# Performance work log

Hardware: AMD Instinct MI355X
Metric: run time of the kernel (lower is better)

## Reference

```python
import jax, jax.numpy as jnp
import numpy as np

NEG_INF = -1e30  # used via float('-inf') in original; -inf literal is fine too


def setup_inputs() -> dict:
    key = jax.random.key(0)
    kq, kk, kv = jax.random.split(key, 3)
    b, h, s, d = 2, 32, 2048, 128
    q = jax.random.normal(kq, (b, h, s, d), dtype=jnp.float32)
    k = jax.random.normal(kk, (b, h, s, d), dtype=jnp.float32)
    v = jax.random.normal(kv, (b, h, s, d), dtype=jnp.float32)
    # causal mask, True = masked (matches the module's `~tril` path when mask is None)
    mask = ~jnp.tril(jnp.ones((s, s), dtype=bool))
    attention_mask = jnp.broadcast_to(mask[None, None], (b, 1, s, s))
    return {"query_layer": q, "key_layer": k, "value_layer": v,
            "attention_mask": attention_mask}


def reference(query_layer, key_layer, value_layer, attention_mask):
    b, h, sq, hd = query_layer.shape
    norm_factor = jnp.sqrt(jnp.asarray(hd, dtype=query_layer.dtype))
    # scores: [b, h, sq, sk], computed in fp32 as in the original (.float())
    scores = jnp.einsum('bhqd,bhkd->bhqk', query_layer, key_layer) / norm_factor
    scores = scores.astype(jnp.float32)
    scores = jnp.where(attention_mask, -jnp.inf, scores)
    probs = jax.nn.softmax(scores, axis=-1).astype(value_layer.dtype)
    # context: [b, h, sq, hd]
    ctx = jnp.einsum('bhqk,bhkd->bhqd', probs, value_layer)
    # -> [b, sq, h*hd]
    ctx = jnp.transpose(ctx, (0, 2, 1, 3)).reshape(b, sq, h * hd)
    return ctx
```

## Files before the change

kernel.cpp:

```cpp
#include <hip/hip_runtime.h>
#include <hip/hip_bf16.h>

typedef __attribute__((ext_vector_type(8))) short bf16x8;
typedef __attribute__((ext_vector_type(8))) unsigned short u16x8;
typedef __attribute__((ext_vector_type(4))) float f32x4;

#define S_LEN 2048
#define D_DIM 128
#define BH_NUM 64
#define OUT_W 4096

__device__ __forceinline__ unsigned short f2bf(float f){
  unsigned int u = __float_as_uint(f);
  u += 0x7FFFu + ((u >> 16) & 1u);
  return (unsigned short)(u >> 16);
}

__device__ __forceinline__ short pbf(float f){
  __hip_bfloat16 h = __float2bfloat16(f);
  return *reinterpret_cast<short*>(&h);
}

__device__ __forceinline__ void gl_lds16(const void* g, void* l){
  __builtin_amdgcn_global_load_lds(
      (const __attribute__((address_space(1))) unsigned int*)g,
      (__attribute__((address_space(3))) unsigned int*)l, 16, 0, 0);
}

__global__ __launch_bounds__(256) void conv_fused(
    const float* __restrict__ K, const float* __restrict__ V,
    unsigned short* __restrict__ Kw, unsigned short* __restrict__ Vt){
  __shared__ unsigned short lt2[32][264];
  const int t  = threadIdx.x;
  const int bh = blockIdx.y;
  if (blockIdx.x < 128){
    const size_t base = (size_t)bh * S_LEN * D_DIM + (size_t)blockIdx.x * 2048 + t * 8;
    const float4* p = (const float4*)(K + base);
    float4 a = p[0], b = p[1];
    u16x8 o;
    o[0]=f2bf(a.x); o[1]=f2bf(a.y); o[2]=f2bf(a.z); o[3]=f2bf(a.w);
    o[4]=f2bf(b.x); o[5]=f2bf(b.y); o[6]=f2bf(b.z); o[7]=f2bf(b.w);
    *(u16x8*)(Kw + base) = o;
  } else {
    const int v    = blockIdx.x - 128;
    const int key0 = (v & 7) * 256;
    const int d0   = (v >> 3) * 32;
    const float* src = V + ((size_t)bh * S_LEN + key0 + t) * D_DIM + d0;
    #pragma unroll
    for (int j = 0; j < 8; ++j){
      float4 x = *(const float4*)(src + j * 4);
      lt2[j*4+0][t] = f2bf(x.x);
      lt2[j*4+1][t] = f2bf(x.y);
      lt2[j*4+2][t] = f2bf(x.z);
      lt2[j*4+3][t] = f2bf(x.w);
    }
    __syncthreads();
    #pragma unroll
    for (int uu = 0; uu < 4; ++uu){
      int u  = uu * 256 + t;
      int d  = u >> 5;
      int j8 = u & 31;
      int base = (j8 >> 3) * 64 + ((j8 >> 2) & 1) * 32 + (j8 & 3) * 4;
      ushort4 a = *(const ushort4*)&lt2[d][base];
      ushort4 b = *(const ushort4*)&lt2[d][base + 16];
      u16x8 o = {a.x, a.y, a.z, a.w, b.x, b.y, b.z, b.w};
      *(u16x8*)(Vt + ((size_t)bh * D_DIM + d0 + d) * S_LEN + key0 + j8 * 8) = o;
    }
  }
}

__device__ __forceinline__ void tile_compute64(
    const unsigned short* __restrict__ kb, const unsigned short* __restrict__ vb,
    const bf16x8 (&qf0)[4], const bf16x8 (&qf1)[4],
    f32x4 (&o0)[8], f32x4 (&o1)[8],
    float& l0, float& l1,
    int kvb, int qw0, int qw1, int c, int t4)
{
  const int cx = c & 7;
  f32x4 s0[4], s1[4];
  #pragma unroll
  for (int g = 0; g < 4; ++g){ s0[g] = (f32x4){0,0,0,0}; s1[g] = (f32x4){0,0,0,0}; }
  __builtin_amdgcn_s_setprio(1);
  #pragma unroll
  for (int g = 0; g < 4; ++g){
    const unsigned short* krow = kb + (size_t)(g * 16 + c) * D_DIM;
    #pragma unroll
    for (int ks = 0; ks < 4; ++ks){
      bf16x8 kf = *(const bf16x8*)(krow + (((ks * 4 + t4) ^ cx) * 8));
      s0[g] = __builtin_amdgcn_mfma_f32_16x16x32_bf16(kf, qf0[ks], s0[g], 0, 0, 0);
      s1[g] = __builtin_amdgcn_mfma_f32_16x16x32_bf16(kf, qf1[ks], s1[g], 0, 0, 0);
    }
  }
  __builtin_amdgcn_s_setprio(0);
  if (kvb + 63 > qw0){
    int q = qw0 + c;
    #pragma unroll
    for (int g = 0; g < 4; ++g)
      #pragma unroll
      for (int r = 0; r < 4; ++r)
        if (kvb + g * 16 + t4 * 4 + r > q) s0[g][r] = -1e30f;
  }
  if (kvb + 63 > qw1){
    int q = qw1 + c;
    #pragma unroll
    for (int g = 0; g < 4; ++g)
      #pragma unroll
      for (int r = 0; r < 4; ++r)
        if (kvb + g * 16 + t4 * 4 + r > q) s1[g][r] = -1e30f;
  }
  bf16x8 p0a, p0b, p1a, p1b;
  #pragma unroll
  for (int g = 0; g < 2; ++g)
    #pragma unroll
    for (int r = 0; r < 4; ++r){
      float e0 = exp2f(s0[g][r]); l0 += e0; p0a[g*4+r] = pbf(e0);
      float e1 = exp2f(s1[g][r]); l1 += e1; p1a[g*4+r] = pbf(e1);
    }
  #pragma unroll
  for (int g = 2; g < 4; ++g)
    #pragma unroll
    for (int r = 0; r < 4; ++r){
      float e0 = exp2f(s0[g][r]); l0 += e0; p0b[(g-2)*4+r] = pbf(e0);
      float e1 = exp2f(s1[g][r]); l1 += e1; p1b[(g-2)*4+r] = pbf(e1);
    }
  __builtin_amdgcn_s_setprio(1);
  #pragma unroll
  for (int db = 0; db < 8; ++db){
    const unsigned short* vrow = vb + (size_t)(db * 16 + c) * 64;
    bf16x8 vf0 = *(const bf16x8*)(vrow + ((t4 ^ cx) * 8));
    bf16x8 vf1 = *(const bf16x8*)(vrow + (((4 + t4) ^ cx) * 8));
    o0[db] = __builtin_amdgcn_mfma_f32_16x16x32_bf16(p0a, vf0, o0[db], 0, 0, 0);
    o0[db] = __builtin_amdgcn_mfma_f32_16x16x32_bf16(p0b, vf1, o0[db], 0, 0, 0);
    o1[db] = __builtin_amdgcn_mfma_f32_16x16x32_bf16(p1a, vf0, o1[db], 0, 0, 0);
    o1[db] = __builtin_amdgcn_mfma_f32_16x16x32_bf16(p1b, vf1, o1[db], 0, 0, 0);
  }
  __builtin_amdgcn_s_setprio(0);
}

__global__ __launch_bounds__(256, 2) void attn_fwd_bf16(
    const float* __restrict__ Qg, const unsigned short* __restrict__ Kw,
    const unsigned short* __restrict__ Vw, float* __restrict__ Og)
{
  __shared__ unsigned short Kl[2][64 * 128];
  __shared__ unsigned short Vl[2][128 * 64];

  const int tid  = threadIdx.x;
  const int lane = tid & 63;
  const int w    = tid >> 6;
  const int c    = lane & 15;
  const int t4   = lane >> 4;
  const int bh   = blockIdx.x;
  const int tq   = 15 - blockIdx.y;
  const unsigned short* Kbh = Kw + (size_t)bh * S_LEN * D_DIM;
  const unsigned short* Vbh = Vw + (size_t)bh * S_LEN * D_DIM;
  const float* Qbh = Qg + (size_t)bh * S_LEN * D_DIM;
  const int bi = bh >> 5, hh = bh & 31;
  const float QS = 0.12751743f;

  const int q0  = tq * 128;
  const int qw0 = q0 + 32 * w;
  const int qw1 = qw0 + 16;

  bf16x8 qf0[4], qf1[4];
  {
    const float* r0 = Qbh + (size_t)(qw0 + c) * D_DIM + t4 * 8;
    const float* r1 = Qbh + (size_t)(qw1 + c) * D_DIM + t4 * 8;
    #pragma unroll
    for (int ks = 0; ks < 4; ++ks){
      float4 a = *(const float4*)(r0 + ks * 32);
      float4 b = *(const float4*)(r0 + ks * 32 + 4);
      bf16x8 f;
      f[0]=pbf(a.x*QS); f[1]=pbf(a.y*QS); f[2]=pbf(a.z*QS); f[3]=pbf(a.w*QS);
      f[4]=pbf(b.x*QS); f[5]=pbf(b.y*QS); f[6]=pbf(b.z*QS); f[7]=pbf(b.w*QS);
      qf0[ks] = f;
      a = *(const float4*)(r1 + ks * 32);
      b = *(const float4*)(r1 + ks * 32 + 4);
      f[0]=pbf(a.x*QS); f[1]=pbf(a.y*QS); f[2]=pbf(a.z*QS); f[3]=pbf(a.w*QS);
      f[4]=pbf(b.x*QS); f[5]=pbf(b.y*QS); f[6]=pbf(b.z*QS); f[7]=pbf(b.w*QS);
      qf1[ks] = f;
    }
  }

  f32x4 o0[8], o1[8];
  #pragma unroll
  for (int db = 0; db < 8; ++db){ o0[db] = (f32x4){0,0,0,0}; o1[db] = (f32x4){0,0,0,0}; }
  float l0 = 0.f, l1 = 0.f;

  const int c1 = tid + 256, c2 = tid + 512, c3 = tid + 768;
  const unsigned short* ka = Kbh + (size_t)(tid >> 4) * D_DIM + (((tid & 15) ^ ((tid >> 4) & 7)) * 8);
  const unsigned short* kb_ = Kbh + (size_t)(c1 >> 4) * D_DIM + (((c1 & 15) ^ ((c1 >> 4) & 7)) * 8);
  const unsigned short* kc = Kbh + (size_t)(c2 >> 4) * D_DIM + (((c2 & 15) ^ ((c2 >> 4) & 7)) * 8);
  const unsigned short* kd = Kbh + (size_t)(c3 >> 4) * D_DIM + (((c3 & 15) ^ ((c3 >> 4) & 7)) * 8);
  const unsigned short* va = Vbh + (size_t)(tid >> 3) * S_LEN + (((tid & 7) ^ ((tid >> 3) & 7)) * 8);
  const unsigned short* vb_ = Vbh + (size_t)(c1 >> 3) * S_LEN + (((c1 & 7) ^ ((c1 >> 3) & 7)) * 8);
  const unsigned short* vc = Vbh + (size_t)(c2 >> 3) * S_LEN + (((c2 & 7) ^ ((c2 >> 3) & 7)) * 8);
  const unsigned short* vd = Vbh + (size_t)(c3 >> 3) * S_LEN + (((c3 & 7) ^ ((c3 >> 3) & 7)) * 8);
  const int du0 = w * 512, du1 = 2048 + w * 512, du2 = 4096 + w * 512, du3 = 6144 + w * 512;

  #define STAGE(KB, VB) do { \
      gl_lds16(ka, (KB) + du0); gl_lds16(kb_, (KB) + du1); \
      gl_lds16(kc, (KB) + du2); gl_lds16(kd, (KB) + du3); \
      gl_lds16(va, (VB) + du0); gl_lds16(vb_, (VB) + du1); \
      gl_lds16(vc, (VB) + du2); gl_lds16(vd, (VB) + du3); \
      ka += 64 * D_DIM; kb_ += 64 * D_DIM; kc += 64 * D_DIM; kd += 64 * D_DIM; \
      va += 64; vb_ += 64; vc += 64; vd += 64; } while(0)

  const int nt   = 2 * tq + 2;
  const int kmax = qw0 + 31;

  STAGE(Kl[0], Vl[0]);
  for (int it = 0; it < nt; it += 2){
    __syncthreads();
    STAGE(Kl[1], Vl[1]);
    if (it * 64 <= kmax)
      tile_compute64(Kl[0], Vl[0], qf0, qf1, o0, o1, l0, l1,
                     it * 64, qw0, qw1, c, t4);
    __syncthreads();
    if (it + 2 < nt)
      STAGE(Kl[0], Vl[0]);
    if ((it + 1) * 64 <= kmax)
      tile_compute64(Kl[1], Vl[1], qf0, qf1, o0, o1, l0, l1,
                     (it + 1) * 64, qw0, qw1, c, t4);
  }
  #undef STAGE

  l0 += __shfl_xor(l0, 16); l0 += __shfl_xor(l0, 32);
  l1 += __shfl_xor(l1, 16); l1 += __shfl_xor(l1, 32);
  float* ob0 = Og + ((size_t)bi * S_LEN + qw0) * OUT_W + hh * D_DIM;
  float* ob1 = Og + ((size_t)bi * S_LEN + qw1) * OUT_W + hh * D_DIM;
  #pragma unroll
  for (int r = 0; r < 4; ++r){
    float lr0 = __shfl(l0, t4 * 4 + r), lr1 = __shfl(l1, t4 * 4 + r);
    float i0 = 1.0f / lr0, i1 = 1.0f / lr1;
    float* w0 = ob0 + (size_t)(t4 * 4 + r) * OUT_W;
    float* w1 = ob1 + (size_t)(t4 * 4 + r) * OUT_W;
    #pragma unroll
    for (int db = 0; db < 8; ++db){
      w0[db * 16 + c] = o0[db][r] * i0;
      w1[db * 16 + c] = o1[db][r] * i1;
    }
  }
}

__global__ __launch_bounds__(256) void attn_fwd(
    const float* __restrict__ Qg, const float* __restrict__ Kg,
    const float* __restrict__ Vg, float* __restrict__ Og)
{
  __shared__ unsigned short Kfb[32][136];
  __shared__ unsigned short Vfb[128][40];
  const int tid  = threadIdx.x;
  const int lane = tid & 63;
  const int w    = tid >> 6;
  const int c    = lane & 15;
  const int t4   = lane >> 4;
  const int q0 = blockIdx.x * 64;
  const int bh = blockIdx.y;
  const size_t base = (size_t)bh * S_LEN * D_DIM;
  const float* Qp = Qg + base;
  const float* Kp = Kg + base;
  const float* Vp = Vg + base;
  const int qw = q0 + w * 16;
  const float QSCALE = 0.08838834764831845f;
  bf16x8 qf[4];
  {
    const float* qrow = Qp + (size_t)(qw + c) * D_DIM + t4 * 8;
    #pragma unroll
    for (int ks = 0; ks < 4; ++ks){
      float4 a = *(const float4*)(qrow + ks * 32);
      float4 b = *(const float4*)(qrow + ks * 32 + 4);
      bf16x8 f;
      f[0]=(short)f2bf(a.x*QSCALE); f[1]=(short)f2bf(a.y*QSCALE);
      f[2]=(short)f2bf(a.z*QSCALE); f[3]=(short)f2bf(a.w*QSCALE);
      f[4]=(short)f2bf(b.x*QSCALE); f[5]=(short)f2bf(b.y*QSCALE);
      f[6]=(short)f2bf(b.z*QSCALE); f[7]=(short)f2bf(b.w*QSCALE);
      qf[ks] = f;
    }
  }
  f32x4 o[8];
  #pragma unroll
  for (int db = 0; db < 8; ++db) o[db] = (f32x4){0.f,0.f,0.f,0.f};
  float m_run = -1e30f, l_run = 0.f;
  const int ntiles = q0 / 32 + 2;
  for (int it = 0; it < ntiles; ++it){
    const int kvb = it * 32;
    #pragma unroll
    for (int rr = 0; rr < 4; ++rr){
      int f   = rr * 256 + tid;
      int key = f >> 5;
      int d0  = (f & 31) * 4;
      float4 k4 = *(const float4*)(Kp + (size_t)(kvb + key) * D_DIM + d0);
      ushort4 pk;
      pk.x = f2bf(k4.x); pk.y = f2bf(k4.y); pk.z = f2bf(k4.z); pk.w = f2bf(k4.w);
      *(ushort4*)&Kfb[key][d0] = pk;
      float4 v4 = *(const float4*)(Vp + (size_t)(kvb + key) * D_DIM + d0);
      int kp = ((key & 15) >> 2) * 8 + (key >> 4) * 4 + (key & 3);
      Vfb[d0 + 0][kp] = f2bf(v4.x);
      Vfb[d0 + 1][kp] = f2bf(v4.y);
      Vfb[d0 + 2][kp] = f2bf(v4.z);
      Vfb[d0 + 3][kp] = f2bf(v4.w);
    }
    __syncthreads();
    if (kvb <= qw + 15){
      f32x4 sg[2];
      #pragma unroll
      for (int g = 0; g < 2; ++g){
        f32x4 acc = (f32x4){0.f,0.f,0.f,0.f};
        #pragma unroll
        for (int ks = 0; ks < 4; ++ks){
          bf16x8 kf = *(const bf16x8*)&Kfb[g*16 + c][ks*32 + t4*8];
          acc = __builtin_amdgcn_mfma_f32_16x16x32_bf16(kf, qf[ks], acc, 0, 0, 0);
        }
        sg[g] = acc;
      }
      if (kvb + 31 > qw){
        int q = qw + c;
        #pragma unroll
        for (int g = 0; g < 2; ++g)
          #pragma unroll
          for (int r = 0; r < 4; ++r){
            int key = kvb + g*16 + t4*4 + r;
            if (key > q) sg[g][r] = -1e30f;
          }
      }
      float mt = sg[0][0];
      #pragma unroll
      for (int g = 0; g < 2; ++g)
        #pragma unroll
        for (int r = 0; r < 4; ++r) mt = fmaxf(mt, sg[g][r]);
      mt = fmaxf(mt, __shfl_xor(mt, 16));
      mt = fmaxf(mt, __shfl_xor(mt, 32));
      float m_new = fmaxf(m_run, mt);
      float alpha = __expf(m_run - m_new);
      m_run = m_new;
      float p[8];
      float rs = 0.f;
      #pragma unroll
      for (int i = 0; i < 8; ++i){
        p[i] = __expf(sg[i>>2][i&3] - m_new);
        rs += p[i];
      }
      rs += __shfl_xor(rs, 16);
      rs += __shfl_xor(rs, 32);
      l_run = l_run * alpha + rs;
      bf16x8 pf;
      #pragma unroll
      for (int i = 0; i < 8; ++i) pf[i] = (short)f2bf(p[i]);
      float a_out[4];
      #pragma unroll
      for (int r = 0; r < 4; ++r) a_out[r] = __shfl(alpha, t4*4 + r);
      #pragma unroll
      for (int db = 0; db < 8; ++db){
        #pragma unroll
        for (int r = 0; r < 4; ++r) o[db][r] *= a_out[r];
      }
      #pragma unroll
      for (int db = 0; db < 8; ++db){
        bf16x8 vf = *(const bf16x8*)&Vfb[db*16 + c][t4*8];
        o[db] = __builtin_amdgcn_mfma_f32_16x16x32_bf16(pf, vf, o[db], 0, 0, 0);
      }
    }
    __syncthreads();
  }
  const int bi = bh >> 5;
  const int hfb = bh & 31;
  float* obase = Og + ((size_t)bi * S_LEN + qw) * OUT_W + hfb * D_DIM;
  #pragma unroll
  for (int r = 0; r < 4; ++r){
    float lrr = __shfl(l_run, t4*4 + r);
    float inv = 1.0f / lrr;
    float* orow = obase + (size_t)(t4*4 + r) * OUT_W;
    #pragma unroll
    for (int db = 0; db < 8; ++db)
      orow[db*16 + c] = o[db][r] * inv;
  }
}

extern "C" void kernel_launch(void* const* d_in, const int* in_sizes, int n_in,
                              void* d_out, int out_size, void* d_ws, size_t ws_size,
                              hipStream_t stream)
{
  const float* Q = (const float*)d_in[0];
  const float* K = (const float*)d_in[1];
  const float* V = (const float*)d_in[2];
  float* O = (float*)d_out;
  const size_t elems = (size_t)BH_NUM * S_LEN * D_DIM;
  const size_t need  = elems * 2 * 2;
  if (ws_size >= need){
    unsigned short* Kw = (unsigned short*)d_ws;
    unsigned short* Vt = Kw + elems;
    conv_fused<<<dim3(128 + 32, BH_NUM), 256, 0, stream>>>(K, V, Kw, Vt);
    attn_fwd_bf16<<<dim3(BH_NUM, 16), 256, 0, stream>>>(Q, Kw, Vt, O);
  } else {
    attn_fwd<<<dim3(S_LEN / 64, BH_NUM), 256, 0, stream>>>(Q, K, V, O);
  }
}
```

Measured before the change: 132.6 us.

## Enlarge query tile to 256 rows per block and balance causal work order

Each wave now processes 64 query rows (four 16-row groups) instead of 32, so a block covers 256 queries and each staged K/V tile is reused across twice as many MFMAs. The grid shrinks from 16 to 8 query blocks per head, and blockIdx.y is remapped so heavy and light causal blocks interleave. This halves K/V traffic from global memory into LDS. In exchange it roughly doubles accumulator and Q-fragment register use, which with launch_bounds(256,2) risks spills or lower occupancy, and leaves fewer, larger blocks, which can hurt load balance.

```diff
diff --git a/kernel.cpp b/kernel.cpp
--- a/kernel.cpp
+++ b/kernel.cpp
@@ -69,17 +69,17 @@
   }
 }
 
-__device__ __forceinline__ void tile_compute64(
+__device__ __forceinline__ void tile_compute256(
     const unsigned short* __restrict__ kb, const unsigned short* __restrict__ vb,
-    const bf16x8 (&qf0)[4], const bf16x8 (&qf1)[4],
-    f32x4 (&o0)[8], f32x4 (&o1)[8],
-    float& l0, float& l1,
-    int kvb, int qw0, int qw1, int c, int t4)
+    const bf16x8 (&qf)[4][4], f32x4 (&o)[4][8], float (&l)[4],
+    int kvb, int qww, int c, int t4)
 {
   const int cx = c & 7;
-  f32x4 s0[4], s1[4];
-  #pragma unroll
-  for (int g = 0; g < 4; ++g){ s0[g] = (f32x4){0,0,0,0}; s1[g] = (f32x4){0,0,0,0}; }
+  f32x4 s[4][4];
+  #pragma unroll
+  for (int qg = 0; qg < 4; ++qg)
+    #pragma unroll
+    for (int g = 0; g < 4; ++g) s[qg][g] = (f32x4){0,0,0,0};
   __builtin_amdgcn_s_setprio(1);
   #pragma unroll
   for (int g = 0; g < 4; ++g){
@@ -87,52 +87,51 @@
     #pragma unroll
     for (int ks = 0; ks < 4; ++ks){
       bf16x8 kf = *(const bf16x8*)(krow + (((ks * 4 + t4) ^ cx) * 8));
-      s0[g] = __builtin_amdgcn_mfma_f32_16x16x32_bf16(kf, qf0[ks], s0[g], 0, 0, 0);
-      s1[g] = __builtin_amdgcn_mfma_f32_16x16x32_bf16(kf, qf1[ks], s1[g], 0, 0, 0);
+      #pragma unroll
+      for (int qg = 0; qg < 4; ++qg)
+        s[qg][g] = __builtin_amdgcn_mfma_f32_16x16x32_bf16(kf, qf[qg][ks], s[qg][g], 0, 0, 0);
     }
   }
   __builtin_amdgcn_s_setprio(0);
-  if (kvb + 63 > qw0){
-    int q = qw0 + c;
-    #pragma unroll
-    for (int g = 0; g < 4; ++g)
-      #pragma unroll
-      for (int r = 0; r < 4; ++r)
-        if (kvb + g * 16 + t4 * 4 + r > q) s0[g][r] = -1e30f;
-  }
-  if (kvb + 63 > qw1){
-    int q = qw1 + c;
-    #pragma unroll
-    for (int g = 0; g < 4; ++g)
-      #pragma unroll
-      for (int r = 0; r < 4; ++r)
-        if (kvb + g * 16 + t4 * 4 + r > q) s1[g][r] = -1e30f;
-  }
-  bf16x8 p0a, p0b, p1a, p1b;
-  #pragma unroll
-  for (int g = 0; g < 2; ++g)
-    #pragma unroll
-    for (int r = 0; r < 4; ++r){
-      float e0 = exp2f(s0[g][r]); l0 += e0; p0a[g*4+r] = pbf(e0);
-      float e1 = exp2f(s1[g][r]); l1 += e1; p1a[g*4+r] = pbf(e1);
-    }
-  #pragma unroll
-  for (int g = 2; g < 4; ++g)
-    #pragma unroll
-    for (int r = 0; r < 4; ++r){
-      float e0 = exp2f(s0[g][r]); l0 += e0; p0b[(g-2)*4+r] = pbf(e0);
-      float e1 = exp2f(s1[g][r]); l1 += e1; p1b[(g-2)*4+r] = pbf(e1);
-    }
+  #pragma unroll
+  for (int qg = 0; qg < 4; ++qg){
+    const int qwg = qww + 16 * qg;
+    if (kvb + 63 > qwg){
+      int q = qwg + c;
+      #pragma unroll
+      for (int g = 0; g < 4; ++g)
+        #pragma unroll
+        for (int r = 0; r < 4; ++r)
+          if (kvb + g * 16 + t4 * 4 + r > q) s[qg][g][r] = -1e30f;
+    }
+  }
+  bf16x8 pa[4], pb[4];
+  #pragma unroll
+  for (int qg = 0; qg < 4; ++qg){
+    #pragma unroll
+    for (int g = 0; g < 2; ++g)
+      #pragma unroll
+      for (int r = 0; r < 4; ++r){
+        float e = exp2f(s[qg][g][r]); l[qg] += e; pa[qg][g*4+r] = pbf(e);
+      }
+    #pragma unroll
+    for (int g = 2; g < 4; ++g)
+      #pragma unroll
+      for (int r = 0; r < 4; ++r){
+        float e = exp2f(s[qg][g][r]); l[qg] += e; pb[qg][(g-2)*4+r] = pbf(e);
+      }
+  }
   __builtin_amdgcn_s_setprio(1);
   #pragma unroll
   for (int db = 0; db < 8; ++db){
     const unsigned short* vrow = vb + (size_t)(db * 16 + c) * 64;
     bf16x8 vf0 = *(const bf16x8*)(vrow + ((t4 ^ cx) * 8));
     bf16x8 vf1 = *(const bf16x8*)(vrow + (((4 + t4) ^ cx) * 8));
-    o0[db] = __builtin_amdgcn_mfma_f32_16x16x32_bf16(p0a, vf0, o0[db], 0, 0, 0);
-    o0[db] = __builtin_amdgcn_mfma_f32_16x16x32_bf16(p0b, vf1, o0[db], 0, 0, 0);
-    o1[db] = __builtin_amdgcn_mfma_f32_16x16x32_bf16(p1a, vf0, o1[db], 0, 0, 0);
-    o1[db] = __builtin_amdgcn_mfma_f32_16x16x32_bf16(p1b, vf1, o1[db], 0, 0, 0);
+    #pragma unroll
+    for (int qg = 0; qg < 4; ++qg){
+      o[qg][db] = __builtin_amdgcn_mfma_f32_16x16x32_bf16(pa[qg], vf0, o[qg][db], 0, 0, 0);
+      o[qg][db] = __builtin_amdgcn_mfma_f32_16x16x32_bf16(pb[qg], vf1, o[qg][db], 0, 0, 0);
+    }
   }
   __builtin_amdgcn_s_setprio(0);
 }
@@ -150,21 +149,22 @@
   const int c    = lane & 15;
   const int t4   = lane >> 4;
   const int bh   = blockIdx.x;
-  const int tq   = 15 - blockIdx.y;
+  const int y    = blockIdx.y;
+  const int bsw  = ((y & 1) << 1) | ((y >> 1) & 1);
+  const int tq   = (y < 4) ? (7 - bsw) : bsw;
   const unsigned short* Kbh = Kw + (size_t)bh * S_LEN * D_DIM;
   const unsigned short* Vbh = Vw + (size_t)bh * S_LEN * D_DIM;
   const float* Qbh = Qg + (size_t)bh * S_LEN * D_DIM;
   const int bi = bh >> 5, hh = bh & 31;
   const float QS = 0.12751743f;
 
-  const int q0  = tq * 128;
-  const int qw0 = q0 + 32 * w;
-  const int qw1 = qw0 + 16;
-
-  bf16x8 qf0[4], qf1[4];
-  {
-    const float* r0 = Qbh + (size_t)(qw0 + c) * D_DIM + t4 * 8;
-    const float* r1 = Qbh + (size_t)(qw1 + c) * D_DIM + t4 * 8;
+  const int q0  = tq * 256;
+  const int qww = q0 + 64 * w;
+
+  bf16x8 qf[4][4];
+  #pragma unroll
+  for (int qg = 0; qg < 4; ++qg){
+    const float* r0 = Qbh + (size_t)(qww + 16 * qg + c) * D_DIM + t4 * 8;
     #pragma unroll
     for (int ks = 0; ks < 4; ++ks){
       float4 a = *(const float4*)(r0 + ks * 32);
@@ -172,19 +172,18 @@
       bf16x8 f;
       f[0]=pbf(a.x*QS); f[1]=pbf(a.y*QS); f[2]=pbf(a.z*QS); f[3]=pbf(a.w*QS);
       f[4]=pbf(b.x*QS); f[5]=pbf(b.y*QS); f[6]=pbf(b.z*QS); f[7]=pbf(b.w*QS);
-      qf0[ks] = f;
-      a = *(const float4*)(r1 + ks * 32);
-      b = *(const float4*)(r1 + ks * 32 + 4);
-      f[0]=pbf(a.x*QS); f[1]=pbf(a.y*QS); f[2]=pbf(a.z*QS); f[3]=pbf(a.w*QS);
-      f[4]=pbf(b.x*QS); f[5]=pbf(b.y*QS); f[6]=pbf(b.z*QS); f[7]=pbf(b.w*QS);
-      qf1[ks] = f;
-    }
-  }
-
-  f32x4 o0[8], o1[8];
-  #pragma unroll
-  for (int db = 0; db < 8; ++db){ o0[db] = (f32x4){0,0,0,0}; o1[db] = (f32x4){0,0,0,0}; }
-  float l0 = 0.f, l1 = 0.f;
+      qf[qg][ks] = f;
+    }
+  }
+
+  f32x4 o[4][8];
+  float l[4];
+  #pragma unroll
+  for (int qg = 0; qg < 4; ++qg){
+    l[qg] = 0.f;
+    #pragma unroll
+    for (int db = 0; db < 8; ++db) o[qg][db] = (f32x4){0,0,0,0};
+  }
 
   const int c1 = tid + 256, c2 = tid + 512, c3 = tid + 768;
   const unsigned short* ka = Kbh + (size_t)(tid >> 4) * D_DIM + (((tid & 15) ^ ((tid >> 4) & 7)) * 8);
@@ -205,39 +204,36 @@
       ka += 64 * D_DIM; kb_ += 64 * D_DIM; kc += 64 * D_DIM; kd += 64 * D_DIM; \
       va += 64; vb_ += 64; vc += 64; vd += 64; } while(0)
 
-  const int nt   = 2 * tq + 2;
-  const int kmax = qw0 + 31;
+  const int nt   = 4 * tq + 4;
+  const int kmax = qww + 63;
 
   STAGE(Kl[0], Vl[0]);
   for (int it = 0; it < nt; it += 2){
     __syncthreads();
     STAGE(Kl[1], Vl[1]);
     if (it * 64 <= kmax)
-      tile_compute64(Kl[0], Vl[0], qf0, qf1, o0, o1, l0, l1,
-                     it * 64, qw0, qw1, c, t4);
+      tile_compute256(Kl[0], Vl[0], qf, o, l, it * 64, qww, c, t4);
     __syncthreads();
     if (it + 2 < nt)
       STAGE(Kl[0], Vl[0]);
     if ((it + 1) * 64 <= kmax)
-      tile_compute64(Kl[1], Vl[1], qf0, qf1, o0, o1, l0, l1,
-                     (it + 1) * 64, qw0, qw1, c, t4);
+      tile_compute256(Kl[1], Vl[1], qf, o, l, (it + 1) * 64, qww, c, t4);
   }
   #undef STAGE
 
-  l0 += __shfl_xor(l0, 16); l0 += __shfl_xor(l0, 32);
-  l1 += __shfl_xor(l1, 16); l1 += __shfl_xor(l1, 32);
-  float* ob0 = Og + ((size_t)bi * S_LEN + qw0) * OUT_W + hh * D_DIM;
-  float* ob1 = Og + ((size_t)bi * S_LEN + qw1) * OUT_W + hh * D_DIM;
-  #pragma unroll
-  for (int r = 0; r < 4; ++r){
-    float lr0 = __shfl(l0, t4 * 4 + r), lr1 = __shfl(l1, t4 * 4 + r);
-    float i0 = 1.0f / lr0, i1 = 1.0f / lr1;
-    float* w0 = ob0 + (size_t)(t4 * 4 + r) * OUT_W;
-    float* w1 = ob1 + (size_t)(t4 * 4 + r) * OUT_W;
-    #pragma unroll
-    for (int db = 0; db < 8; ++db){
-      w0[db * 16 + c] = o0[db][r] * i0;
-      w1[db * 16 + c] = o1[db][r] * i1;
+  #pragma unroll
+  for (int qg = 0; qg < 4; ++qg){
+    l[qg] += __shfl_xor(l[qg], 16);
+    l[qg] += __shfl_xor(l[qg], 32);
+    float* ob = Og + ((size_t)bi * S_LEN + qww + 16 * qg) * OUT_W + hh * D_DIM;
+    #pragma unroll
+    for (int r = 0; r < 4; ++r){
+      float lr = __shfl(l[qg], t4 * 4 + r);
+      float iv = 1.0f / lr;
+      float* w0 = ob + (size_t)(t4 * 4 + r) * OUT_W;
+      #pragma unroll
+      for (int db = 0; db < 8; ++db)
+        w0[db * 16 + c] = o[qg][db][r] * iv;
     }
   }
 }
@@ -389,7 +385,7 @@
     unsigned short* Kw = (unsigned short*)d_ws;
     unsigned short* Vt = Kw + elems;
     conv_fused<<<dim3(128 + 32, BH_NUM), 256, 0, stream>>>(K, V, Kw, Vt);
-    attn_fwd_bf16<<<dim3(BH_NUM, 16), 256, 0, stream>>>(Q, Kw, Vt, O);
+    attn_fwd_bf16<<<dim3(BH_NUM, 8), 256, 0, stream>>>(Q, Kw, Vt, O);
   } else {
     attn_fwd<<<dim3(S_LEN / 64, BH_NUM), 256, 0, stream>>>(Q, K, V, O);
   }
```

Result: slower. 332.7 us (+150.9%).
